# Kernel tuning notes

Measured on AMD Instinct MI355X. Metric: run time of the kernel, lower is better.

Reference implementation:

```python
import jax, jax.numpy as jnp
import numpy as np

N = 100000
SEQ = 12
DIMS = [32, 64, 64, 32]


def _glorot(key, shape):
    fan_in, fan_out = shape[0], shape[1]
    lim = jnp.sqrt(6.0 / (fan_in + fan_out))
    return jax.random.uniform(key, shape, jnp.float32, -lim, lim)


def setup_inputs() -> dict:
    key = jax.random.key(0)
    ks = jax.random.split(key, 8)
    x = jax.random.normal(ks[0], (N, DIMS[0], 1), dtype=jnp.float32)
    spiral_indices = jax.random.randint(ks[1], (N, SEQ), 0, N)
    # SpiralConv i: Linear(SEQ * DIMS[i], DIMS[i+1])
    W0 = _glorot(ks[2], (SEQ * DIMS[0], DIMS[1]))
    b0 = jnp.zeros((DIMS[1],), jnp.float32)
    W1 = _glorot(ks[3], (SEQ * DIMS[1], DIMS[2]))
    b1 = jnp.zeros((DIMS[2],), jnp.float32)
    W2 = _glorot(ks[4], (SEQ * DIMS[2], DIMS[3]))
    b2 = jnp.zeros((DIMS[3],), jnp.float32)
    return {"x": x, "spiral_indices": spiral_indices,
            "W0": W0, "b0": b0, "W1": W1, "b1": b1, "W2": W2, "b2": b2}


def _spiral_conv(h, idx, W, b):
    # h: [N, C]; idx: [N, SEQ] -> gathered [N, SEQ, C] -> flat [N, SEQ*C]
    n = h.shape[0]
    g = jnp.take(h, idx, axis=0).reshape(n, -1)
    return g @ W + b


def reference(x, spiral_indices, W0, b0, W1, b1, W2, b2):
    h = x[..., 0]  # squeeze(-1): [N, C_in]
    h = jax.nn.elu(_spiral_conv(h, spiral_indices, W0, b0))
    h = jax.nn.elu(_spiral_conv(h, spiral_indices, W1, b1))
    h = _spiral_conv(h, spiral_indices, W2, b2)  # final_activation=False
    return h[:, :, None]
```

## Files before the change

kernel.cpp:

```cpp
#include <hip/hip_runtime.h>
#include <math.h>


typedef __bf16 bf16;
typedef bf16  bf16x4 __attribute__((ext_vector_type(4)));
typedef bf16  bf16x8 __attribute__((ext_vector_type(8)));
typedef float f32x4  __attribute__((ext_vector_type(4)));

template<int CIN, int COUT>
__device__ inline void pack_one(const float* __restrict__ W, bf16* __restrict__ BP, int e) {
    constexpr int NT = COUT / 16, CC = CIN / 32;
    const int f = e >> 9, r = e & 511, lane = r >> 3, j = r & 7;
    const int t = f % NT, cc = (f / NT) % CC, s = f / (NT * CC);
    const int col = t * 16 + (lane & 15);
    const int k   = s * CIN + cc * 32 + (lane >> 4) * 8 + j;
    BP[e] = (bf16)W[k * COUT + col];
}

__global__ __launch_bounds__(256)
void prep_all(const float* __restrict__ x, bf16* __restrict__ xb,
              const float* __restrict__ W0, const float* __restrict__ W1,
              const float* __restrict__ W2, bf16* __restrict__ B0,
              bf16* __restrict__ B1, bf16* __restrict__ B2, int n)
{
    const int gid = blockIdx.x * 256 + threadIdx.x;
    const int e = gid * 4;
    if (e < n * 32) {
        const f32x4 v = *reinterpret_cast<const f32x4*>(x + e);
        bf16x4 o = {(bf16)v[0], (bf16)v[1], (bf16)v[2], (bf16)v[3]};
        *reinterpret_cast<bf16x4*>(xb + e) = o;
    }
    if (gid < 384 * 64)                       pack_one<32, 64>(W0, B0, gid);
    else if (gid < 384 * 64 + 768 * 64)       pack_one<64, 64>(W1, B1, gid - 384 * 64);
    else if (gid < 384 * 64 + 768 * 64 + 768 * 32)
                                              pack_one<64, 32>(W2, B2, gid - 384 * 64 - 768 * 64);
}

template<int CIN, int COUT, bool ELU, typename TOUT>
__global__ __launch_bounds__(256, 3)
void spiral_mfma(const bf16* __restrict__ h, const int* __restrict__ idx,
                 const bf16* __restrict__ BP, const float* __restrict__ bias,
                 TOUT* __restrict__ out, int n)
{
    constexpr int CC = CIN / 32;
    constexpr int NT = COUT / 16;
    constexpr int PS = CIN * COUT;
    constexpr int SC = (24576 / PS < 12) ? (24576 / PS) : 12;
    constexpr int NCH = 12 / SC;

    __shared__ bf16 Bs[SC * PS];

    const int tid  = threadIdx.x;
    const int lane = tid & 63;
    const int wave = tid >> 6;
    const int m    = lane & 15;
    const int quad = lane >> 4;
    const int i0   = (blockIdx.x * 4 + wave) * 32;
    const bool valid = (i0 < n);

    int rg0[12], rg1[12];
    if (valid) {
        const int4* p0 = reinterpret_cast<const int4*>(idx + (size_t)(i0 + m) * 12);
        const int4* p1 = reinterpret_cast<const int4*>(idx + (size_t)(i0 + 16 + m) * 12);
        const int4 q00 = p0[0], q01 = p0[1], q02 = p0[2];
        const int4 q10 = p1[0], q11 = p1[1], q12 = p1[2];
        rg0[0]=q00.x; rg0[1]=q00.y; rg0[2]=q00.z; rg0[3]=q00.w;
        rg0[4]=q01.x; rg0[5]=q01.y; rg0[6]=q01.z; rg0[7]=q01.w;
        rg0[8]=q02.x; rg0[9]=q02.y; rg0[10]=q02.z; rg0[11]=q02.w;
        rg1[0]=q10.x; rg1[1]=q10.y; rg1[2]=q10.z; rg1[3]=q10.w;
        rg1[4]=q11.x; rg1[5]=q11.y; rg1[6]=q11.z; rg1[7]=q11.w;
        rg1[8]=q12.x; rg1[9]=q12.y; rg1[10]=q12.z; rg1[11]=q12.w;
    }

    f32x4 acc0[NT] = {}, acc1[NT] = {};

    #pragma unroll
    for (int c = 0; c < NCH; ++c) {
        if (c) __syncthreads();
        const bf16* src = BP + (size_t)c * SC * PS;
        #pragma unroll
        for (int r2 = tid; r2 < SC * PS / 8; r2 += 256)
            *reinterpret_cast<bf16x8*>(&Bs[r2 * 8]) =
                *reinterpret_cast<const bf16x8*>(&src[r2 * 8]);
        __syncthreads();

        if (valid) {
            #pragma unroll
            for (int sl = 0; sl < SC; ++sl) {
                const int s = c * SC + sl;
                #pragma unroll
                for (int cc = 0; cc < CC; ++cc) {
                    const int co = cc * 32 + quad * 8;
                    const bf16x8 a0 = *reinterpret_cast<const bf16x8*>(
                        h + (size_t)rg0[s] * CIN + co);
                    const bf16x8 a1 = *reinterpret_cast<const bf16x8*>(
                        h + (size_t)rg1[s] * CIN + co);
                    #pragma unroll
                    for (int t = 0; t < NT; ++t) {
                        const bf16x8 b = *reinterpret_cast<const bf16x8*>(
                            &Bs[((sl * CC + cc) * NT + t) * 512 + lane * 8]);
                        acc0[t] = __builtin_amdgcn_mfma_f32_16x16x32_bf16(a0, b, acc0[t], 0, 0, 0);
                        acc1[t] = __builtin_amdgcn_mfma_f32_16x16x32_bf16(a1, b, acc1[t], 0, 0, 0);
                    }
                }
            }
        }
    }

    if (!valid) return;

    #pragma unroll
    for (int t = 0; t < NT; ++t) {
        const int col = t * 16 + m;
        const float bv = bias[col];
        #pragma unroll
        for (int g = 0; g < 4; ++g) {
            {
                const int row = i0 + quad * 4 + g;
                float v = acc0[t][g] + bv;
                if (ELU) v = (v > 0.f) ? v : (__expf(v) - 1.f);
                out[(size_t)row * COUT + col] = (TOUT)v;
            }
            {
                const int row = i0 + 16 + quad * 4 + g;
                float v = acc1[t][g] + bv;
                if (ELU) v = (v > 0.f) ? v : (__expf(v) - 1.f);
                out[(size_t)row * COUT + col] = (TOUT)v;
            }
        }
    }
}

extern "C" void kernel_launch(void* const* d_in, const int* in_sizes, int n_in,
                              void* d_out, int out_size, void* d_ws, size_t ws_size,
                              hipStream_t stream) {
    const float* x   = (const float*)d_in[0];
    const int*   idx = (const int*)d_in[1];
    const float* W0  = (const float*)d_in[2];
    const float* b0  = (const float*)d_in[3];
    const float* W1  = (const float*)d_in[4];
    const float* b1  = (const float*)d_in[5];
    const float* W2  = (const float*)d_in[6];
    const float* b2  = (const float*)d_in[7];
    float* out = (float*)d_out;

    const int n = in_sizes[0] / 32;

    bf16* xb = (bf16*)d_ws;
    bf16* h1 = xb + (size_t)n * 32;
    bf16* h2 = h1 + (size_t)n * 64;
    bf16* B0 = h2 + (size_t)n * 64;
    bf16* B1 = B0 + 384 * 64;
    bf16* B2 = B1 + 768 * 64;

    dim3 blk(256);
    const int prep_threads = n * 8;
    prep_all<<<(prep_threads + 255) / 256, blk, 0, stream>>>(x, xb, W0, W1, W2, B0, B1, B2, n);

    const int grid = (n + 127) / 128;
    spiral_mfma<32, 64, true,  bf16 ><<<grid, blk, 0, stream>>>(xb, idx, B0, b0, h1,  n);
    spiral_mfma<64, 64, true,  bf16 ><<<grid, blk, 0, stream>>>(h1, idx, B1, b1, h2,  n);
    spiral_mfma<64, 32, false, float><<<grid, blk, 0, stream>>>(h2, idx, B2, b2, out, n);
}
```

Baseline: 177.2 us.

## Batch gathered A-loads per chunk and shrink blocks to two waves

The spiral conv kernel now issues all gathered row loads for a chunk into register arrays before running the MFMA loop, so the global gathers are in flight together instead of interleaved with compute. Blocks drop from four waves to two, and the weight chunk in shared memory is resized to six 32-wide k-slices per chunk. Index loads are clamped instead of guarded, so every lane runs uniformly. The goal is more memory-level parallelism and more resident blocks, at the cost of more registers for the staged A fragments and more chunk barriers per block.

```diff
diff --git a/kernel.cpp b/kernel.cpp
--- a/kernel.cpp
+++ b/kernel.cpp
@@ -37,16 +37,17 @@
 }
 
 template<int CIN, int COUT, bool ELU, typename TOUT>
-__global__ __launch_bounds__(256, 3)
+__global__ __launch_bounds__(128, 3)
 void spiral_mfma(const bf16* __restrict__ h, const int* __restrict__ idx,
                  const bf16* __restrict__ BP, const float* __restrict__ bias,
                  TOUT* __restrict__ out, int n)
 {
-    constexpr int CC = CIN / 32;
-    constexpr int NT = COUT / 16;
-    constexpr int PS = CIN * COUT;
-    constexpr int SC = (24576 / PS < 12) ? (24576 / PS) : 12;
+    constexpr int CC  = CIN / 32;
+    constexpr int NT  = COUT / 16;
+    constexpr int PS  = CIN * COUT;
+    constexpr int SC  = 6 / CC;
     constexpr int NCH = 12 / SC;
+    constexpr int PL  = SC * CC;
 
     __shared__ bf16 Bs[SC * PS];
 
@@ -55,22 +56,17 @@
     const int wave = tid >> 6;
     const int m    = lane & 15;
     const int quad = lane >> 4;
-    const int i0   = (blockIdx.x * 4 + wave) * 32;
+    const int i0   = (blockIdx.x * 2 + wave) * 32;
     const bool valid = (i0 < n);
 
-    int rg0[12], rg1[12];
-    if (valid) {
-        const int4* p0 = reinterpret_cast<const int4*>(idx + (size_t)(i0 + m) * 12);
-        const int4* p1 = reinterpret_cast<const int4*>(idx + (size_t)(i0 + 16 + m) * 12);
-        const int4 q00 = p0[0], q01 = p0[1], q02 = p0[2];
-        const int4 q10 = p1[0], q11 = p1[1], q12 = p1[2];
-        rg0[0]=q00.x; rg0[1]=q00.y; rg0[2]=q00.z; rg0[3]=q00.w;
-        rg0[4]=q01.x; rg0[5]=q01.y; rg0[6]=q01.z; rg0[7]=q01.w;
-        rg0[8]=q02.x; rg0[9]=q02.y; rg0[10]=q02.z; rg0[11]=q02.w;
-        rg1[0]=q10.x; rg1[1]=q10.y; rg1[2]=q10.z; rg1[3]=q10.w;
-        rg1[4]=q11.x; rg1[5]=q11.y; rg1[6]=q11.z; rg1[7]=q11.w;
-        rg1[8]=q12.x; rg1[9]=q12.y; rg1[10]=q12.z; rg1[11]=q12.w;
-    }
+    const int ir0 = min(i0 + m,      n - 1);
+    const int ir1 = min(i0 + 16 + m, n - 1);
+    const int4* p0 = reinterpret_cast<const int4*>(idx + (size_t)ir0 * 12);
+    const int4* p1 = reinterpret_cast<const int4*>(idx + (size_t)ir1 * 12);
+    const int4 q00 = p0[0], q01 = p0[1], q02 = p0[2];
+    const int4 q10 = p1[0], q11 = p1[1], q12 = p1[2];
+    const int rg0[12] = {q00.x,q00.y,q00.z,q00.w, q01.x,q01.y,q01.z,q01.w, q02.x,q02.y,q02.z,q02.w};
+    const int rg1[12] = {q10.x,q10.y,q10.z,q10.w, q11.x,q11.y,q11.z,q11.w, q12.x,q12.y,q12.z,q12.w};
 
     f32x4 acc0[NT] = {}, acc1[NT] = {};
 
@@ -79,30 +75,33 @@
         if (c) __syncthreads();
         const bf16* src = BP + (size_t)c * SC * PS;
         #pragma unroll
-        for (int r2 = tid; r2 < SC * PS / 8; r2 += 256)
+        for (int r2 = tid; r2 < SC * PS / 8; r2 += 128)
             *reinterpret_cast<bf16x8*>(&Bs[r2 * 8]) =
                 *reinterpret_cast<const bf16x8*>(&src[r2 * 8]);
         __syncthreads();
 
-        if (valid) {
+        bf16x8 a0[PL], a1[PL];
+        #pragma unroll
+        for (int sl = 0; sl < SC; ++sl) {
+            const int s = c * SC + sl;
             #pragma unroll
-            for (int sl = 0; sl < SC; ++sl) {
-                const int s = c * SC + sl;
-                #pragma unroll
-                for (int cc = 0; cc < CC; ++cc) {
-                    const int co = cc * 32 + quad * 8;
-                    const bf16x8 a0 = *reinterpret_cast<const bf16x8*>(
-                        h + (size_t)rg0[s] * CIN + co);
-                    const bf16x8 a1 = *reinterpret_cast<const bf16x8*>(
-                        h + (size_t)rg1[s] * CIN + co);
-                    #pragma unroll
-                    for (int t = 0; t < NT; ++t) {
-                        const bf16x8 b = *reinterpret_cast<const bf16x8*>(
-                            &Bs[((sl * CC + cc) * NT + t) * 512 + lane * 8]);
-                        acc0[t] = __builtin_amdgcn_mfma_f32_16x16x32_bf16(a0, b, acc0[t], 0, 0, 0);
-                        acc1[t] = __builtin_amdgcn_mfma_f32_16x16x32_bf16(a1, b, acc1[t], 0, 0, 0);
-                    }
-                }
+            for (int cc = 0; cc < CC; ++cc) {
+                const int co = cc * 32 + quad * 8;
+                a0[sl * CC + cc] = *reinterpret_cast<const bf16x8*>(
+                    h + (size_t)rg0[s] * CIN + co);
+                a1[sl * CC + cc] = *reinterpret_cast<const bf16x8*>(
+                    h + (size_t)rg1[s] * CIN + co);
+            }
+        }
+
+        #pragma unroll
+        for (int p = 0; p < PL; ++p) {
+            #pragma unroll
+            for (int t = 0; t < NT; ++t) {
+                const bf16x8 b = *reinterpret_cast<const bf16x8*>(
+                    &Bs[(p * NT + t) * 512 + lane * 8]);
+                acc0[t] = __builtin_amdgcn_mfma_f32_16x16x32_bf16(a0[p], b, acc0[t], 0, 0, 0);
+                acc1[t] = __builtin_amdgcn_mfma_f32_16x16x32_bf16(a1[p], b, acc1[t], 0, 0, 0);
             }
         }
     }
@@ -153,12 +152,11 @@
     bf16* B1 = B0 + 384 * 64;
     bf16* B2 = B1 + 768 * 64;
 
-    dim3 blk(256);
     const int prep_threads = n * 8;
-    prep_all<<<(prep_threads + 255) / 256, blk, 0, stream>>>(x, xb, W0, W1, W2, B0, B1, B2, n);
+    prep_all<<<(prep_threads + 255) / 256, dim3(256), 0, stream>>>(x, xb, W0, W1, W2, B0, B1, B2, n);
 
-    const int grid = (n + 127) / 128;
-    spiral_mfma<32, 64, true,  bf16 ><<<grid, blk, 0, stream>>>(xb, idx, B0, b0, h1,  n);
-    spiral_mfma<64, 64, true,  bf16 ><<<grid, blk, 0, stream>>>(h1, idx, B1, b1, h2,  n);
-    spiral_mfma<64, 32, false, float><<<grid, blk, 0, stream>>>(h2, idx, B2, b2, out, n);
+    const int grid = (n + 63) / 64;
+    spiral_mfma<32, 64, true,  bf16 ><<<grid, dim3(128), 0, stream>>>(xb, idx, B0, b0, h1,  n);
+    spiral_mfma<64, 64, true,  bf16 ><<<grid, dim3(128), 0, stream>>>(h1, idx, B1, b1, h2,  n);
+    spiral_mfma<64, 32, false, float><<<grid, dim3(128), 0, stream>>>(h2, idx, B2, b2, out, n);
 }
```

Result: slower. 187.5 us (+5.8%).
